# Kernel optimization log

Measured on AMD Instinct MI355X. Metric: run time of the kernel, lower is better.

The kernel has to match this reference:

```python
import jax, jax.numpy as jnp
import numpy as np

B, T, D = 512, 256, 64
LATENT = 128
H = 2 * LATENT  # hidden size = latent_dim * 2


def setup_inputs() -> dict:
    key = jax.random.key(0)
    ks = jax.random.split(key, 16)
    x = jax.random.normal(ks[0], (B, T, D), dtype=jnp.float32)
    # strictly increasing time points
    tps = jnp.cumsum(jax.random.uniform(ks[1], (T,), dtype=jnp.float32, minval=0.01, maxval=0.1))
    # ragged mask: each trajectory observed for a random prefix length in [1, T]
    lengths = jax.random.randint(ks[2], (B,), 1, T + 1)
    mask = (jnp.arange(T)[None, :] < lengths[:, None]).astype(jnp.float32)
    s = 0.05
    # GRUCell params (torch layout: gates ordered r, z, n)
    w_ih = jax.random.normal(ks[3], (3 * H, D), dtype=jnp.float32) * s
    w_hh = jax.random.normal(ks[4], (3 * H, H), dtype=jnp.float32) * s
    b_ih = jax.random.normal(ks[5], (3 * H,), dtype=jnp.float32) * s
    b_hh = jax.random.normal(ks[6], (3 * H,), dtype=jnp.float32) * s
    # Neural ODE func: Linear -> tanh -> Linear
    w1 = jax.random.normal(ks[7], (H, H), dtype=jnp.float32) * s
    b1 = jax.random.normal(ks[8], (H,), dtype=jnp.float32) * s
    w2 = jax.random.normal(ks[9], (H, H), dtype=jnp.float32) * s
    b2 = jax.random.normal(ks[10], (H,), dtype=jnp.float32) * s
    # output linear
    w_out = jax.random.normal(ks[11], (H, H), dtype=jnp.float32) * s
    b_out = jax.random.normal(ks[12], (H,), dtype=jnp.float32) * s
    return {"x": x, "tps": tps, "mask": mask, "w_ih": w_ih, "w_hh": w_hh,
            "b_ih": b_ih, "b_hh": b_hh, "w1": w1, "b1": b1, "w2": w2,
            "b2": b2, "w_out": w_out, "b_out": b_out}


def _gru_ode_forward(x, tps, mask, w_ih, w_hh, b_ih, b_hh, w1, b1, w2, b2, w_out, b_out):
    Bn, Tn, _ = x.shape
    # right_fill_mask: 1 wherever some earlier timestep (strictly before j) was observed
    r_fill = ((jnp.cumsum(mask, axis=1) - mask) > 0).astype(x.dtype)  # (B,T)
    # Euler dt per step; dt[0] is unused (r_fill[:,0]==0 forces h_ode=h at i=0)
    dt = jnp.diff(tps, prepend=tps[:1] - 0.01)  # (T,)

    def node_f(h):
        return jnp.tanh(h @ w1.T + b1) @ w2.T + b2

    def gru_cell(x_t, h):
        gi = x_t @ w_ih.T + b_ih
        gh = h @ w_hh.T + b_hh
        gi_r, gi_z, gi_n = jnp.split(gi, 3, axis=-1)
        gh_r, gh_z, gh_n = jnp.split(gh, 3, axis=-1)
        r = jax.nn.sigmoid(gi_r + gh_r)
        z = jax.nn.sigmoid(gi_z + gh_z)
        n = jnp.tanh(gi_n + r * gh_n)
        return (1.0 - z) * n + z * h

    def step(h, inp):
        x_t, dt_t, m_t, r_t = inp  # (B,D), (), (B,), (B,)
        h_euler = h + dt_t * node_f(h)          # single Euler step
        r_c = r_t[:, None]
        h_ode = h_euler * r_c + h * (1.0 - r_c)  # freeze state before first obs
        h_rnn = gru_cell(x_t, h_ode)
        m_c = m_t[:, None]
        h_new = h_rnn * m_c + h_ode * (1.0 - m_c)  # update only at observations
        return h_new, h_new

    h0 = jnp.zeros((Bn, H), dtype=x.dtype)
    xs = (jnp.swapaxes(x, 0, 1), dt, mask.T, r_fill.T)
    _, h_arr = jax.lax.scan(step, h0, xs)  # (T,B,H)
    # last observed timestep per trajectory
    ind = (Tn - 1) - jnp.argmax(mask[:, ::-1], axis=1)  # (B,)
    h_last = h_arr[ind, jnp.arange(Bn)]  # (B,H)
    return h_last @ w_out.T + b_out


def reference(x, tps, mask, w_ih, w_hh, b_ih, b_hh, w1, b1, w2, b2, w_out, b_out):
    return _gru_ode_forward(x, tps, mask, w_ih, w_hh, b_ih, b_hh, w1, b1, w2, b2, w_out, b_out)
```

## Files before the change

kernel.cpp:

```cpp
#include <hip/hip_runtime.h>
#include <hip/hip_bf16.h>


#define Bn 512
#define Tn 256
#define Dn 64
#define Hn 256

typedef __bf16 bf16x8 __attribute__((ext_vector_type(8)));
typedef float f32x4 __attribute__((ext_vector_type(4)));

__device__ __forceinline__ f32x4 mfma_bf16(bf16x8 a, bf16x8 b, f32x4 c) {
  return __builtin_amdgcn_mfma_f32_16x16x32_bf16(a, b, c, 0, 0, 0);
}
__device__ __forceinline__ float fast_sigmoid(float x) {
  return __builtin_amdgcn_rcpf(1.0f + __expf(-x));
}
__device__ __forceinline__ float fast_tanh(float x) {
  return 1.0f - 2.0f * __builtin_amdgcn_rcpf(1.0f + __expf(2.0f * x));
}

__global__ void pack_w(const float* __restrict__ w, __bf16* __restrict__ out,
                       int N, int K) {
  int idx = blockIdx.x * blockDim.x + threadIdx.x;
  if (idx >= N * K) return;
  int n = idx / K, k = idx % K;
  int tile = n >> 4, kb = k >> 5;
  int lane = (n & 15) + (((k & 31) >> 3) << 4);
  int j = k & 7;
  out[(((tile * (K >> 5) + kb) << 6) + lane) * 8 + j] = (__bf16)w[idx];
}

__global__ void pack_w_hilo(const float* __restrict__ w, __bf16* __restrict__ hi,
                            __bf16* __restrict__ lo, int N, int K) {
  int idx = blockIdx.x * blockDim.x + threadIdx.x;
  if (idx >= N * K) return;
  int n = idx / K, k = idx % K;
  int tile = n >> 4, kb = k >> 5;
  int lane = (n & 15) + (((k & 31) >> 3) << 4);
  int j = k & 7;
  int o = (((tile * (K >> 5) + kb) << 6) + lane) * 8 + j;
  float f = w[idx];
  __bf16 h = (__bf16)f;
  hi[o] = h;
  lo[o] = (__bf16)(f - (float)h);
}

__launch_bounds__(512)
__global__ void gru_ode_kernel(
    const float* __restrict__ x, const float* __restrict__ tps,
    const float* __restrict__ mask,
    const float* __restrict__ b_ih, const float* __restrict__ b_hh,
    const float* __restrict__ b1, const float* __restrict__ b2,
    const float* __restrict__ b_out,
    const __bf16* __restrict__ w1p, const __bf16* __restrict__ w2p,
    const __bf16* __restrict__ whhp, const __bf16* __restrict__ wihp,
    const __bf16* __restrict__ wouth, const __bf16* __restrict__ woutl,
    float* __restrict__ out) {
  __shared__ __align__(16) __bf16 h_fr[4096];
  __shared__ __align__(16) __bf16 a_fr[4096];
  __shared__ __align__(16) __bf16 o_fr[4096];
  __shared__ __align__(16) __bf16 wih_l[49152];
  __shared__ __align__(16) float hlast[16][260];
  __shared__ float tps_s[Tn];
  __shared__ int len_s[16];
  __shared__ int maxlen_s;

  const int tid = threadIdx.x;
  const int wv = tid >> 6;
  const int l = tid & 63;
  const int g = l >> 4;
  const int c = l & 15;
  const int m0 = blockIdx.x << 4;

  if (tid < Tn) tps_s[tid] = tps[tid];
#pragma unroll
  for (int i = 0; i < 8; i++) o_fr[tid + i * 512] = (__bf16)0.0f;
  {
    const int4* s4 = (const int4*)wihp;
    int4* d4 = (int4*)wih_l;
    for (int i = tid; i < 6144; i += 512) d4[i] = s4[i];
  }
  {
    int m = tid >> 5, l32 = tid & 31;
    const float* mr = mask + (size_t)(m0 + m) * Tn + l32 * 8;
    float s = 0.f;
#pragma unroll
    for (int i = 0; i < 8; i++) s += mr[i];
#pragma unroll
    for (int o = 16; o; o >>= 1) s += __shfl_down(s, o, 32);
    if (l32 == 0) len_s[m] = (int)(s + 0.5f);
  }
  __syncthreads();
  if (tid == 0) {
    int mx = 1;
    for (int i = 0; i < 16; i++) mx = max(mx, len_s[i]);
    maxlen_s = mx;
  }
  __syncthreads();
  const int maxlen = maxlen_s;
  int len4[4];
#pragma unroll
  for (int r = 0; r < 4; r++) len4[r] = len_s[4 * g + r];

  float bb1[2], bb2[2], brz[4], bin[2], bhn[2], bo[2];
#pragma unroll
  for (int nt = 0; nt < 2; nt++) {
    int col = 32 * wv + 16 * nt + c;
    bb1[nt] = b1[col];
    bb2[nt] = b2[col];
    brz[nt] = b_ih[col] + b_hh[col];
    brz[2 + nt] = b_ih[256 + col] + b_hh[256 + col];
    bin[nt] = b_ih[512 + col];
    bhn[nt] = b_hh[512 + col];
    bo[nt] = b_out[col];
  }

  float hreg[2][4] = {{0, 0, 0, 0}, {0, 0, 0, 0}};

  const bf16x8* w1f = (const bf16x8*)w1p;
  const bf16x8* w2f = (const bf16x8*)w2p;
  const bf16x8* whf = (const bf16x8*)whhp;
  const bf16x8* wif = (const bf16x8*)wih_l;

  const int wbase = (wv * 64 + 4 * g + 16 * (c >> 3)) * 8 + (c & 7);

  for (int t = 0; t < maxlen; t++) {
    const float* xp = x + (size_t)(m0 + c) * (Tn * Dn) + t * Dn + 8 * g;
    f32x4 xr0 = *(const f32x4*)(xp);
    f32x4 xr1 = *(const f32x4*)(xp + 4);
    f32x4 xr2 = *(const f32x4*)(xp + 32);
    f32x4 xr3 = *(const f32x4*)(xp + 36);

    if (t > 0) {
      bf16x8 hf[8];
#pragma unroll
      for (int kb = 0; kb < 8; kb++) hf[kb] = *(const bf16x8*)&h_fr[(kb * 64 + l) * 8];
#pragma unroll
      for (int nt = 0; nt < 2; nt++) {
        f32x4 acc = {0.f, 0.f, 0.f, 0.f};
#pragma unroll
        for (int kb = 0; kb < 8; kb++)
          acc = mfma_bf16(hf[kb], w1f[((2 * wv + nt) * 8 + kb) * 64 + l], acc);
#pragma unroll
        for (int r = 0; r < 4; r++)
          a_fr[wbase + (r + 32 * nt) * 8] = (__bf16)fast_tanh(acc[r] + bb1[nt]);
      }
      __syncthreads();
      float dtv = tps_s[t] - tps_s[t - 1];
      bf16x8 af[8];
#pragma unroll
      for (int kb = 0; kb < 8; kb++) af[kb] = *(const bf16x8*)&a_fr[(kb * 64 + l) * 8];
#pragma unroll
      for (int nt = 0; nt < 2; nt++) {
        f32x4 acc = {0.f, 0.f, 0.f, 0.f};
#pragma unroll
        for (int kb = 0; kb < 8; kb++)
          acc = mfma_bf16(af[kb], w2f[((2 * wv + nt) * 8 + kb) * 64 + l], acc);
#pragma unroll
        for (int r = 0; r < 4; r++) {
          hreg[nt][r] += dtv * (acc[r] + bb2[nt]);
          o_fr[wbase + (r + 32 * nt) * 8] = (__bf16)hreg[nt][r];
        }
      }
      __syncthreads();
    }
    bf16x8 of[8];
#pragma unroll
    for (int kb = 0; kb < 8; kb++) of[kb] = *(const bf16x8*)&o_fr[(kb * 64 + l) * 8];
    bf16x8 xf0, xf1;
#pragma unroll
    for (int j = 0; j < 4; j++) {
      xf0[j] = (__bf16)xr0[j]; xf0[4 + j] = (__bf16)xr1[j];
      xf1[j] = (__bf16)xr2[j]; xf1[4 + j] = (__bf16)xr3[j];
    }
    f32x4 arz[4], agi[2], agh[2];
#pragma unroll
    for (int q = 0; q < 4; q++) {
      int gate = q >> 1, nt = q & 1;
      int tile = (gate << 4) + 2 * wv + nt;
      f32x4 acc = {0.f, 0.f, 0.f, 0.f};
      acc = mfma_bf16(xf0, wif[(tile * 2 + 0) * 64 + l], acc);
      acc = mfma_bf16(xf1, wif[(tile * 2 + 1) * 64 + l], acc);
#pragma unroll
      for (int kb = 0; kb < 8; kb++)
        acc = mfma_bf16(of[kb], whf[(tile * 8 + kb) * 64 + l], acc);
      arz[q] = acc;
    }
#pragma unroll
    for (int nt = 0; nt < 2; nt++) {
      int tile = 32 + 2 * wv + nt;
      f32x4 ai = {0.f, 0.f, 0.f, 0.f}, ah = {0.f, 0.f, 0.f, 0.f};
      ai = mfma_bf16(xf0, wif[(tile * 2 + 0) * 64 + l], ai);
      ai = mfma_bf16(xf1, wif[(tile * 2 + 1) * 64 + l], ai);
#pragma unroll
      for (int kb = 0; kb < 8; kb++)
        ah = mfma_bf16(of[kb], whf[(tile * 8 + kb) * 64 + l], ah);
      agi[nt] = ai;
      agh[nt] = ah;
    }
#pragma unroll
    for (int nt = 0; nt < 2; nt++) {
#pragma unroll
      for (int r = 0; r < 4; r++) {
        float rg = fast_sigmoid(arz[nt][r] + brz[nt]);
        float zg = fast_sigmoid(arz[2 + nt][r] + brz[2 + nt]);
        float ng = fast_tanh(agi[nt][r] + bin[nt] + rg * (agh[nt][r] + bhn[nt]));
        float hn = (1.f - zg) * ng + zg * hreg[nt][r];
        hreg[nt][r] = hn;
        if (t == len4[r] - 1) hlast[4 * g + r][32 * wv + 16 * nt + c] = hn;
        h_fr[wbase + (r + 32 * nt) * 8] = (__bf16)hn;
      }
    }
    __syncthreads();
  }

  const bf16x8* woh = (const bf16x8*)wouth;
  const bf16x8* wol = (const bf16x8*)woutl;
  f32x4 oa[2] = {{0.f, 0.f, 0.f, 0.f}, {0.f, 0.f, 0.f, 0.f}};
#pragma unroll
  for (int kb = 0; kb < 8; kb++) {
    f32x4 v0 = *(const f32x4*)&hlast[c][kb * 32 + 8 * g];
    f32x4 v1 = *(const f32x4*)&hlast[c][kb * 32 + 8 * g + 4];
    bf16x8 hhi, hlo;
#pragma unroll
    for (int j = 0; j < 4; j++) {
      __bf16 p = (__bf16)v0[j]; hhi[j] = p; hlo[j] = (__bf16)(v0[j] - (float)p);
      __bf16 q = (__bf16)v1[j]; hhi[4 + j] = q; hlo[4 + j] = (__bf16)(v1[j] - (float)q);
    }
#pragma unroll
    for (int nt = 0; nt < 2; nt++) {
      int tile = 2 * wv + nt;
      oa[nt] = mfma_bf16(hhi, woh[(tile * 8 + kb) * 64 + l], oa[nt]);
      oa[nt] = mfma_bf16(hlo, woh[(tile * 8 + kb) * 64 + l], oa[nt]);
      oa[nt] = mfma_bf16(hhi, wol[(tile * 8 + kb) * 64 + l], oa[nt]);
    }
  }
#pragma unroll
  for (int nt = 0; nt < 2; nt++)
#pragma unroll
    for (int r = 0; r < 4; r++)
      out[(size_t)(m0 + 4 * g + r) * Hn + 32 * wv + 16 * nt + c] = oa[nt][r] + bo[nt];
}

extern "C" void kernel_launch(void* const* d_in, const int* in_sizes, int n_in,
                              void* d_out, int out_size, void* d_ws, size_t ws_size,
                              hipStream_t stream) {
  const float* x = (const float*)d_in[0];
  const float* tps = (const float*)d_in[1];
  const float* mask = (const float*)d_in[2];
  const float* w_ih = (const float*)d_in[3];
  const float* w_hh = (const float*)d_in[4];
  const float* b_ih = (const float*)d_in[5];
  const float* b_hh = (const float*)d_in[6];
  const float* w1 = (const float*)d_in[7];
  const float* b1 = (const float*)d_in[8];
  const float* w2 = (const float*)d_in[9];
  const float* b2 = (const float*)d_in[10];
  const float* w_out = (const float*)d_in[11];
  const float* b_out = (const float*)d_in[12];

  char* ws = (char*)d_ws;
  __bf16* w1p = (__bf16*)(ws + 0);
  __bf16* w2p = (__bf16*)(ws + 131072);
  __bf16* whhp = (__bf16*)(ws + 262144);
  __bf16* wihp = (__bf16*)(ws + 655360);
  __bf16* wouth = (__bf16*)(ws + 753664);
  __bf16* woutl = (__bf16*)(ws + 884736);

  pack_w<<<(256 * 256 + 255) / 256, 256, 0, stream>>>(w1, w1p, 256, 256);
  pack_w<<<(256 * 256 + 255) / 256, 256, 0, stream>>>(w2, w2p, 256, 256);
  pack_w<<<(768 * 256 + 255) / 256, 256, 0, stream>>>(w_hh, whhp, 768, 256);
  pack_w<<<(768 * 64 + 255) / 256, 256, 0, stream>>>(w_ih, wihp, 768, 64);
  pack_w_hilo<<<(256 * 256 + 255) / 256, 256, 0, stream>>>(w_out, wouth, woutl, 256, 256);

  gru_ode_kernel<<<32, 512, 0, stream>>>(x, tps, mask, b_ih, b_hh, b1, b2, b_out,
                                         w1p, w2p, whhp, wihp, wouth, woutl,
                                         (float*)d_out);
}
```

Measured before the change: 2.875 ms.

## Stream GRU weights through LDS ring via async global_load_lds, keep ODE weights in registers

Keeps W1/W2 fragments resident in registers instead of reloading them from global memory each step. W_hh and W_ih are streamed every timestep through a three-slot LDS ring using global_load_lds, with manual vmcnt waits. The x tile for the next step is prefetched into a double-buffered LDS buffer. Barriers are replaced with raw s_barrier plus lgkmcnt waits, and launch bounds request two blocks per CU. This trades heavier register pressure and fragile hand-written wait counts for overlapping the weight loads with MFMA work.

```diff
diff --git a/kernel.cpp b/kernel.cpp
--- a/kernel.cpp
+++ b/kernel.cpp
@@ -18,6 +18,11 @@
 }
 __device__ __forceinline__ float fast_tanh(float x) {
   return 1.0f - 2.0f * __builtin_amdgcn_rcpf(1.0f + __expf(2.0f * x));
+}
+
+__device__ __forceinline__ void gld16(const void* g, void* l) {
+  __builtin_amdgcn_global_load_lds((const __attribute__((address_space(1))) void*)g,
+                                   (__attribute__((address_space(3))) void*)l, 16, 0, 0);
 }
 
 __global__ void pack_w(const float* __restrict__ w, __bf16* __restrict__ out,
@@ -46,7 +51,43 @@
   lo[o] = (__bf16)(f - (float)h);
 }
 
-__launch_bounds__(512)
+#define RING_WAIT()                                          \
+  asm volatile("s_waitcnt vmcnt(8)" ::: "memory");           \
+  __builtin_amdgcn_sched_barrier(0);
+
+#define BAR()                                                \
+  asm volatile("s_waitcnt lgkmcnt(0)" ::: "memory");         \
+  __builtin_amdgcn_sched_barrier(0);                         \
+  __builtin_amdgcn_s_barrier();                              \
+  __builtin_amdgcn_sched_barrier(0);
+
+#define ISSUE_W(k)                                                             \
+  {                                                                            \
+    __bf16* db_ = slots + ((k) % 3) * 16384 + wv * 2048;                       \
+    if ((k) < 12) {                                                            \
+      const int tile_ = ((k) >> 2) * 16 + 2 * wv + (((k) & 3) >> 1);           \
+      const int kb0_ = ((k) & 1) * 4;                                          \
+      _Pragma("unroll") for (int f_ = 0; f_ < 4; f_++)                         \
+          gld16(whh_lane + (tile_ * 8 + kb0_ + f_) * 512, db_ + f_ * 512);     \
+    } else {                                                                   \
+      const int gg_ = (k) - 12;                                                \
+      _Pragma("unroll") for (int f_ = 0; f_ < 4; f_++) {                       \
+        const int tile_ = gg_ * 16 + 2 * wv + (f_ >> 1);                       \
+        gld16(wih_lane + (tile_ * 2 + (f_ & 1)) * 512, db_ + f_ * 512);        \
+      }                                                                        \
+    }                                                                          \
+  }
+
+#define ISSUE_X(tt)                                                            \
+  {                                                                            \
+    const int t2_ = ((tt) < Tn) ? (tt) : Tn - 1;                               \
+    const float* xs_ = x_lane + t2_ * 64;                                      \
+    float* xd_ = &xbuf[(tt) & 1][0];                                           \
+    _Pragma("unroll") for (int f_ = 0; f_ < 4; f_++)                           \
+        gld16(xs_ + f_ * 16, xd_ + f_ * 256);                                  \
+  }
+
+__launch_bounds__(512, 2)
 __global__ void gru_ode_kernel(
     const float* __restrict__ x, const float* __restrict__ tps,
     const float* __restrict__ mask,
@@ -57,12 +98,13 @@
     const __bf16* __restrict__ whhp, const __bf16* __restrict__ wihp,
     const __bf16* __restrict__ wouth, const __bf16* __restrict__ woutl,
     float* __restrict__ out) {
+  __shared__ __align__(16) __bf16 slots[49152];
   __shared__ __align__(16) __bf16 h_fr[4096];
   __shared__ __align__(16) __bf16 a_fr[4096];
   __shared__ __align__(16) __bf16 o_fr[4096];
-  __shared__ __align__(16) __bf16 wih_l[49152];
+  __shared__ __align__(16) float xbuf[2][1024];
   __shared__ __align__(16) float hlast[16][260];
-  __shared__ float tps_s[Tn];
+  __shared__ float dt_s[Tn];
   __shared__ int len_s[16];
   __shared__ int maxlen_s;
 
@@ -73,14 +115,9 @@
   const int c = l & 15;
   const int m0 = blockIdx.x << 4;
 
-  if (tid < Tn) tps_s[tid] = tps[tid];
+  if (tid < Tn) dt_s[tid] = tid ? tps[tid] - tps[tid - 1] : 0.01f;
 #pragma unroll
   for (int i = 0; i < 8; i++) o_fr[tid + i * 512] = (__bf16)0.0f;
-  {
-    const int4* s4 = (const int4*)wihp;
-    int4* d4 = (int4*)wih_l;
-    for (int i = tid; i < 6144; i += 512) d4[i] = s4[i];
-  }
   {
     int m = tid >> 5, l32 = tid & 31;
     const float* mr = mask + (size_t)(m0 + m) * Tn + l32 * 8;
@@ -116,103 +153,142 @@
     bo[nt] = b_out[col];
   }
 
+  bf16x8 w1f[2][8], w2f[2][8];
+#pragma unroll
+  for (int nt = 0; nt < 2; nt++)
+#pragma unroll
+    for (int kb = 0; kb < 8; kb++) {
+      w1f[nt][kb] = *(const bf16x8*)&w1p[(((2 * wv + nt) * 8 + kb) * 64 + l) * 8];
+      w2f[nt][kb] = *(const bf16x8*)&w2p[(((2 * wv + nt) * 8 + kb) * 64 + l) * 8];
+    }
+
   float hreg[2][4] = {{0, 0, 0, 0}, {0, 0, 0, 0}};
 
-  const bf16x8* w1f = (const bf16x8*)w1p;
-  const bf16x8* w2f = (const bf16x8*)w2p;
-  const bf16x8* whf = (const bf16x8*)whhp;
-  const bf16x8* wif = (const bf16x8*)wih_l;
+  const __bf16* whh_lane = whhp + l * 8;
+  const __bf16* wih_lane = wihp + l * 8;
+  const float* x_lane = x + (size_t)(m0 + (l & 15)) * (Tn * Dn) + (l >> 4) * 4;
 
   const int wbase = (wv * 64 + 4 * g + 16 * (c >> 3)) * 8 + (c & 7);
 
+  ISSUE_X(0);
+  asm volatile("s_waitcnt vmcnt(0)" ::: "memory");
+  __builtin_amdgcn_sched_barrier(0);
+  ISSUE_W(0);
+  ISSUE_W(1);
+  ISSUE_W(2);
+
+  bf16x8 xf0, xf1;
+
   for (int t = 0; t < maxlen; t++) {
-    const float* xp = x + (size_t)(m0 + c) * (Tn * Dn) + t * Dn + 8 * g;
-    f32x4 xr0 = *(const f32x4*)(xp);
-    f32x4 xr1 = *(const f32x4*)(xp + 4);
-    f32x4 xr2 = *(const f32x4*)(xp + 32);
-    f32x4 xr3 = *(const f32x4*)(xp + 36);
-
     if (t > 0) {
-      bf16x8 hf[8];
-#pragma unroll
-      for (int kb = 0; kb < 8; kb++) hf[kb] = *(const bf16x8*)&h_fr[(kb * 64 + l) * 8];
-#pragma unroll
-      for (int nt = 0; nt < 2; nt++) {
-        f32x4 acc = {0.f, 0.f, 0.f, 0.f};
+      {
+        bf16x8 hfv[8];
 #pragma unroll
         for (int kb = 0; kb < 8; kb++)
-          acc = mfma_bf16(hf[kb], w1f[((2 * wv + nt) * 8 + kb) * 64 + l], acc);
-#pragma unroll
-        for (int r = 0; r < 4; r++)
-          a_fr[wbase + (r + 32 * nt) * 8] = (__bf16)fast_tanh(acc[r] + bb1[nt]);
-      }
-      __syncthreads();
-      float dtv = tps_s[t] - tps_s[t - 1];
-      bf16x8 af[8];
-#pragma unroll
-      for (int kb = 0; kb < 8; kb++) af[kb] = *(const bf16x8*)&a_fr[(kb * 64 + l) * 8];
-#pragma unroll
-      for (int nt = 0; nt < 2; nt++) {
-        f32x4 acc = {0.f, 0.f, 0.f, 0.f};
+          hfv[kb] = *(const bf16x8*)&h_fr[(kb * 64 + l) * 8];
+#pragma unroll
+        for (int nt = 0; nt < 2; nt++) {
+          f32x4 acc = {0.f, 0.f, 0.f, 0.f};
+#pragma unroll
+          for (int kb = 0; kb < 8; kb++) acc = mfma_bf16(hfv[kb], w1f[nt][kb], acc);
+#pragma unroll
+          for (int r = 0; r < 4; r++)
+            a_fr[wbase + (r + 32 * nt) * 8] = (__bf16)fast_tanh(acc[r] + bb1[nt]);
+        }
+      }
+      BAR();
+      {
+        const float dtv = dt_s[t];
+        bf16x8 afv[8];
 #pragma unroll
         for (int kb = 0; kb < 8; kb++)
-          acc = mfma_bf16(af[kb], w2f[((2 * wv + nt) * 8 + kb) * 64 + l], acc);
-#pragma unroll
-        for (int r = 0; r < 4; r++) {
-          hreg[nt][r] += dtv * (acc[r] + bb2[nt]);
-          o_fr[wbase + (r + 32 * nt) * 8] = (__bf16)hreg[nt][r];
-        }
-      }
-      __syncthreads();
-    }
-    bf16x8 of[8];
-#pragma unroll
-    for (int kb = 0; kb < 8; kb++) of[kb] = *(const bf16x8*)&o_fr[(kb * 64 + l) * 8];
-    bf16x8 xf0, xf1;
-#pragma unroll
-    for (int j = 0; j < 4; j++) {
-      xf0[j] = (__bf16)xr0[j]; xf0[4 + j] = (__bf16)xr1[j];
-      xf1[j] = (__bf16)xr2[j]; xf1[4 + j] = (__bf16)xr3[j];
-    }
-    f32x4 arz[4], agi[2], agh[2];
-#pragma unroll
-    for (int q = 0; q < 4; q++) {
-      int gate = q >> 1, nt = q & 1;
-      int tile = (gate << 4) + 2 * wv + nt;
-      f32x4 acc = {0.f, 0.f, 0.f, 0.f};
-      acc = mfma_bf16(xf0, wif[(tile * 2 + 0) * 64 + l], acc);
-      acc = mfma_bf16(xf1, wif[(tile * 2 + 1) * 64 + l], acc);
-#pragma unroll
-      for (int kb = 0; kb < 8; kb++)
-        acc = mfma_bf16(of[kb], whf[(tile * 8 + kb) * 64 + l], acc);
-      arz[q] = acc;
-    }
+          afv[kb] = *(const bf16x8*)&a_fr[(kb * 64 + l) * 8];
+#pragma unroll
+        for (int nt = 0; nt < 2; nt++) {
+          f32x4 acc = {0.f, 0.f, 0.f, 0.f};
+#pragma unroll
+          for (int kb = 0; kb < 8; kb++) acc = mfma_bf16(afv[kb], w2f[nt][kb], acc);
+#pragma unroll
+          for (int r = 0; r < 4; r++) {
+            hreg[nt][r] += dtv * (acc[r] + bb2[nt]);
+            o_fr[wbase + (r + 32 * nt) * 8] = (__bf16)hreg[nt][r];
+          }
+        }
+      }
+      BAR();
+    }
+
+    f32x4 acc6[6], agi2[2];
+#pragma unroll
+    for (int q = 0; q < 6; q++) acc6[q] = (f32x4){0.f, 0.f, 0.f, 0.f};
+    agi2[0] = (f32x4){0.f, 0.f, 0.f, 0.f};
+    agi2[1] = (f32x4){0.f, 0.f, 0.f, 0.f};
+
+#pragma unroll
+    for (int p = 0; p < 16; p++) {
+      RING_WAIT();
+      if (p == 0) {
+        const float* xb = &xbuf[t & 1][0];
+        f32x4 a0 = *(const f32x4*)&xb[(2 * g) * 64 + c * 4];
+        f32x4 a1 = *(const f32x4*)&xb[(2 * g + 1) * 64 + c * 4];
+        f32x4 b0 = *(const f32x4*)&xb[(8 + 2 * g) * 64 + c * 4];
+        f32x4 b1v = *(const f32x4*)&xb[(9 + 2 * g) * 64 + c * 4];
+#pragma unroll
+        for (int j = 0; j < 4; j++) {
+          xf0[j] = (__bf16)a0[j];
+          xf0[4 + j] = (__bf16)a1[j];
+          xf1[j] = (__bf16)b0[j];
+          xf1[4 + j] = (__bf16)b1v[j];
+        }
+      }
+      if (p < 12) {
+        const int gate = p >> 2, nt = (p & 3) >> 1, kb0 = (p & 1) * 4;
+        const int ai = (gate < 2) ? gate * 2 + nt : 4 + nt;
+        const __bf16* sb = slots + (p % 3) * 16384 + wv * 2048 + l * 8;
+#pragma unroll
+        for (int f = 0; f < 4; f++) {
+          bf16x8 wf = *(const bf16x8*)(sb + f * 512);
+          bf16x8 ofr = *(const bf16x8*)&o_fr[((kb0 + f) * 64 + l) * 8];
+          acc6[ai] = mfma_bf16(ofr, wf, acc6[ai]);
+        }
+      } else if (p < 15) {
+        const int gg = p - 12;
+        const __bf16* sb = slots + (p % 3) * 16384 + wv * 2048 + l * 8;
+#pragma unroll
+        for (int f = 0; f < 4; f++) {
+          bf16x8 wf = *(const bf16x8*)(sb + f * 512);
+          if (gg < 2)
+            acc6[gg * 2 + (f >> 1)] = mfma_bf16((f & 1) ? xf1 : xf0, wf, acc6[gg * 2 + (f >> 1)]);
+          else
+            agi2[f >> 1] = mfma_bf16((f & 1) ? xf1 : xf0, wf, agi2[f >> 1]);
+        }
+      }
+      asm volatile("s_waitcnt lgkmcnt(0)" ::: "memory");
+      __builtin_amdgcn_sched_barrier(0);
+      {
+        const int k = (p + 3) & 15;
+        if (k == 15) {
+          ISSUE_X(t + 1);
+        } else {
+          ISSUE_W(k);
+        }
+      }
+    }
+
 #pragma unroll
     for (int nt = 0; nt < 2; nt++) {
-      int tile = 32 + 2 * wv + nt;
-      f32x4 ai = {0.f, 0.f, 0.f, 0.f}, ah = {0.f, 0.f, 0.f, 0.f};
-      ai = mfma_bf16(xf0, wif[(tile * 2 + 0) * 64 + l], ai);
-      ai = mfma_bf16(xf1, wif[(tile * 2 + 1) * 64 + l], ai);
-#pragma unroll
-      for (int kb = 0; kb < 8; kb++)
-        ah = mfma_bf16(of[kb], whf[(tile * 8 + kb) * 64 + l], ah);
-      agi[nt] = ai;
-      agh[nt] = ah;
-    }
-#pragma unroll
-    for (int nt = 0; nt < 2; nt++) {
 #pragma unroll
       for (int r = 0; r < 4; r++) {
-        float rg = fast_sigmoid(arz[nt][r] + brz[nt]);
-        float zg = fast_sigmoid(arz[2 + nt][r] + brz[2 + nt]);
-        float ng = fast_tanh(agi[nt][r] + bin[nt] + rg * (agh[nt][r] + bhn[nt]));
+        float rg = fast_sigmoid(acc6[nt][r] + brz[nt]);
+        float zg = fast_sigmoid(acc6[2 + nt][r] + brz[2 + nt]);
+        float ng = fast_tanh(agi2[nt][r] + bin[nt] + rg * (acc6[4 + nt][r] + bhn[nt]));
         float hn = (1.f - zg) * ng + zg * hreg[nt][r];
         hreg[nt][r] = hn;
         if (t == len4[r] - 1) hlast[4 * g + r][32 * wv + 16 * nt + c] = hn;
         h_fr[wbase + (r + 32 * nt) * 8] = (__bf16)hn;
       }
     }
-    __syncthreads();
+    BAR();
   }
 
   const bf16x8* woh = (const bf16x8*)wouth;
```

Measured after the change: 2.666 ms. -7.3%, faster.

## Hold ODE weights in registers and double-buffer W_hh prefetch in GRU step

Applied to the files above, without the earlier changes.

Loads the w1/w2 ODE weight fragments into registers once before the time loop instead of fetching them from global memory every step. The recurrent W_hh fragments are streamed in 4-fragment chunks with double-buffered prefetch, so the global loads overlap the MFMA accumulation. __syncthreads is replaced by a custom LDS-wait-plus-barrier macro, dt is precomputed, and launch bounds now request 2 blocks per CU. The cost is much higher register pressure, which may cause spills or lower occupancy.

```diff
diff --git a/kernel.cpp b/kernel.cpp
--- a/kernel.cpp
+++ b/kernel.cpp
@@ -46,7 +46,23 @@
   lo[o] = (__bf16)(f - (float)h);
 }
 
-__launch_bounds__(512)
+#define BAR()                                        \
+  asm volatile("s_waitcnt lgkmcnt(0)" ::: "memory"); \
+  __builtin_amdgcn_sched_barrier(0);                 \
+  __builtin_amdgcn_s_barrier();                      \
+  __builtin_amdgcn_sched_barrier(0);
+
+#define CHUNK_Q(p) (((p) >= 6) ? (p) - 6 : (p))
+#define CHUNK_TILE(p) (((CHUNK_Q(p) >> 1) << 4) + 2 * wv + (CHUNK_Q(p) & 1))
+#define CHUNK_KB0(p) (((p) >= 6) ? 4 : 0)
+#define ISSUE_CHUNK(p, b)                                                  \
+  {                                                                        \
+    const int tl_ = CHUNK_TILE(p), kb_ = CHUNK_KB0(p);                     \
+    _Pragma("unroll") for (int f_ = 0; f_ < 4; f_++)                       \
+        wb[b][f_] = whf[(tl_ * 8 + kb_ + f_) * 64 + l];                    \
+  }
+
+__launch_bounds__(512, 2)
 __global__ void gru_ode_kernel(
     const float* __restrict__ x, const float* __restrict__ tps,
     const float* __restrict__ mask,
@@ -57,12 +73,12 @@
     const __bf16* __restrict__ whhp, const __bf16* __restrict__ wihp,
     const __bf16* __restrict__ wouth, const __bf16* __restrict__ woutl,
     float* __restrict__ out) {
+  __shared__ __align__(16) __bf16 wih_l[49152];
   __shared__ __align__(16) __bf16 h_fr[4096];
   __shared__ __align__(16) __bf16 a_fr[4096];
   __shared__ __align__(16) __bf16 o_fr[4096];
-  __shared__ __align__(16) __bf16 wih_l[49152];
   __shared__ __align__(16) float hlast[16][260];
-  __shared__ float tps_s[Tn];
+  __shared__ float dt_s[Tn];
   __shared__ int len_s[16];
   __shared__ int maxlen_s;
 
@@ -73,7 +89,7 @@
   const int c = l & 15;
   const int m0 = blockIdx.x << 4;
 
-  if (tid < Tn) tps_s[tid] = tps[tid];
+  if (tid < Tn) dt_s[tid] = tid ? tps[tid] - tps[tid - 1] : 0.01f;
 #pragma unroll
   for (int i = 0; i < 8; i++) o_fr[tid + i * 512] = (__bf16)0.0f;
   {
@@ -116,103 +132,130 @@
     bo[nt] = b_out[col];
   }
 
+  bf16x8 w1f[2][8], w2f[2][8];
+#pragma unroll
+  for (int nt = 0; nt < 2; nt++)
+#pragma unroll
+    for (int kb = 0; kb < 8; kb++) {
+      w1f[nt][kb] = *(const bf16x8*)&w1p[(((2 * wv + nt) * 8 + kb) * 64 + l) * 8];
+      w2f[nt][kb] = *(const bf16x8*)&w2p[(((2 * wv + nt) * 8 + kb) * 64 + l) * 8];
+    }
+
   float hreg[2][4] = {{0, 0, 0, 0}, {0, 0, 0, 0}};
 
-  const bf16x8* w1f = (const bf16x8*)w1p;
-  const bf16x8* w2f = (const bf16x8*)w2p;
   const bf16x8* whf = (const bf16x8*)whhp;
-  const bf16x8* wif = (const bf16x8*)wih_l;
+  const bf16x8* wifl = (const bf16x8*)wih_l;
+  const float* xrow = x + (size_t)(m0 + c) * (Tn * Dn) + 8 * g;
 
   const int wbase = (wv * 64 + 4 * g + 16 * (c >> 3)) * 8 + (c & 7);
 
   for (int t = 0; t < maxlen; t++) {
-    const float* xp = x + (size_t)(m0 + c) * (Tn * Dn) + t * Dn + 8 * g;
+    const float* xp = xrow + t * Dn;
     f32x4 xr0 = *(const f32x4*)(xp);
     f32x4 xr1 = *(const f32x4*)(xp + 4);
     f32x4 xr2 = *(const f32x4*)(xp + 32);
     f32x4 xr3 = *(const f32x4*)(xp + 36);
+    bf16x8 wb[2][4];
+    ISSUE_CHUNK(0, 0);
+    ISSUE_CHUNK(1, 1);
 
     if (t > 0) {
-      bf16x8 hf[8];
-#pragma unroll
-      for (int kb = 0; kb < 8; kb++) hf[kb] = *(const bf16x8*)&h_fr[(kb * 64 + l) * 8];
-#pragma unroll
-      for (int nt = 0; nt < 2; nt++) {
-        f32x4 acc = {0.f, 0.f, 0.f, 0.f};
+      {
+        bf16x8 hfv[8];
 #pragma unroll
         for (int kb = 0; kb < 8; kb++)
-          acc = mfma_bf16(hf[kb], w1f[((2 * wv + nt) * 8 + kb) * 64 + l], acc);
-#pragma unroll
-        for (int r = 0; r < 4; r++)
-          a_fr[wbase + (r + 32 * nt) * 8] = (__bf16)fast_tanh(acc[r] + bb1[nt]);
-      }
-      __syncthreads();
-      float dtv = tps_s[t] - tps_s[t - 1];
-      bf16x8 af[8];
-#pragma unroll
-      for (int kb = 0; kb < 8; kb++) af[kb] = *(const bf16x8*)&a_fr[(kb * 64 + l) * 8];
-#pragma unroll
-      for (int nt = 0; nt < 2; nt++) {
-        f32x4 acc = {0.f, 0.f, 0.f, 0.f};
+          hfv[kb] = *(const bf16x8*)&h_fr[(kb * 64 + l) * 8];
+#pragma unroll
+        for (int nt = 0; nt < 2; nt++) {
+          f32x4 acc = {0.f, 0.f, 0.f, 0.f};
+#pragma unroll
+          for (int kb = 0; kb < 8; kb++) acc = mfma_bf16(hfv[kb], w1f[nt][kb], acc);
+#pragma unroll
+          for (int r = 0; r < 4; r++)
+            a_fr[wbase + (r + 32 * nt) * 8] = (__bf16)fast_tanh(acc[r] + bb1[nt]);
+        }
+      }
+      BAR();
+      {
+        const float dtv = dt_s[t];
+        bf16x8 afv[8];
 #pragma unroll
         for (int kb = 0; kb < 8; kb++)
-          acc = mfma_bf16(af[kb], w2f[((2 * wv + nt) * 8 + kb) * 64 + l], acc);
-#pragma unroll
-        for (int r = 0; r < 4; r++) {
-          hreg[nt][r] += dtv * (acc[r] + bb2[nt]);
-          o_fr[wbase + (r + 32 * nt) * 8] = (__bf16)hreg[nt][r];
+          afv[kb] = *(const bf16x8*)&a_fr[(kb * 64 + l) * 8];
+#pragma unroll
+        for (int nt = 0; nt < 2; nt++) {
+          f32x4 acc = {0.f, 0.f, 0.f, 0.f};
+#pragma unroll
+          for (int kb = 0; kb < 8; kb++) acc = mfma_bf16(afv[kb], w2f[nt][kb], acc);
+#pragma unroll
+          for (int r = 0; r < 4; r++) {
+            hreg[nt][r] += dtv * (acc[r] + bb2[nt]);
+            o_fr[wbase + (r + 32 * nt) * 8] = (__bf16)hreg[nt][r];
+          }
         }
       }
-      __syncthreads();
-    }
-    bf16x8 of[8];
-#pragma unroll
-    for (int kb = 0; kb < 8; kb++) of[kb] = *(const bf16x8*)&o_fr[(kb * 64 + l) * 8];
+      BAR();
+    }
+
     bf16x8 xf0, xf1;
 #pragma unroll
     for (int j = 0; j < 4; j++) {
-      xf0[j] = (__bf16)xr0[j]; xf0[4 + j] = (__bf16)xr1[j];
-      xf1[j] = (__bf16)xr2[j]; xf1[4 + j] = (__bf16)xr3[j];
-    }
-    f32x4 arz[4], agi[2], agh[2];
-#pragma unroll
-    for (int q = 0; q < 4; q++) {
-      int gate = q >> 1, nt = q & 1;
-      int tile = (gate << 4) + 2 * wv + nt;
-      f32x4 acc = {0.f, 0.f, 0.f, 0.f};
-      acc = mfma_bf16(xf0, wif[(tile * 2 + 0) * 64 + l], acc);
-      acc = mfma_bf16(xf1, wif[(tile * 2 + 1) * 64 + l], acc);
-#pragma unroll
-      for (int kb = 0; kb < 8; kb++)
-        acc = mfma_bf16(of[kb], whf[(tile * 8 + kb) * 64 + l], acc);
-      arz[q] = acc;
-    }
+      xf0[j] = (__bf16)xr0[j];
+      xf0[4 + j] = (__bf16)xr1[j];
+      xf1[j] = (__bf16)xr2[j];
+      xf1[4 + j] = (__bf16)xr3[j];
+    }
+    f32x4 acc6[6], agi2[2];
+#pragma unroll
+    for (int q = 0; q < 6; q++) acc6[q] = (f32x4){0.f, 0.f, 0.f, 0.f};
+    agi2[0] = (f32x4){0.f, 0.f, 0.f, 0.f};
+    agi2[1] = (f32x4){0.f, 0.f, 0.f, 0.f};
+
+    bf16x8 ofv[4];
+#pragma unroll
+    for (int p = 0; p < 12; p++) {
+      const int kb0 = CHUNK_KB0(p);
+      const int q = CHUNK_Q(p);
+      const int gate = q >> 1, nt = q & 1;
+      if (p == 0 || p == 6) {
+#pragma unroll
+        for (int f = 0; f < 4; f++)
+          ofv[f] = *(const bf16x8*)&o_fr[((kb0 + f) * 64 + l) * 8];
+      }
+      f32x4& accr = (gate == 0) ? acc6[nt] : (gate == 1) ? acc6[2 + nt] : acc6[4 + nt];
+#pragma unroll
+      for (int f = 0; f < 4; f++) accr = mfma_bf16(ofv[f], wb[p & 1][f], accr);
+      if (p < 10) {
+        ISSUE_CHUNK(p + 2, p & 1);
+      }
+    }
+#pragma unroll
+    for (int gg = 0; gg < 3; gg++) {
+#pragma unroll
+      for (int f = 0; f < 4; f++) {
+        const int tile = gg * 16 + 2 * wv + (f >> 1);
+        bf16x8 wf = wifl[(tile * 2 + (f & 1)) * 64 + l];
+        if (gg < 2)
+          acc6[gg * 2 + (f >> 1)] = mfma_bf16((f & 1) ? xf1 : xf0, wf, acc6[gg * 2 + (f >> 1)]);
+        else
+          agi2[f >> 1] = mfma_bf16((f & 1) ? xf1 : xf0, wf, agi2[f >> 1]);
+      }
+    }
+
 #pragma unroll
     for (int nt = 0; nt < 2; nt++) {
-      int tile = 32 + 2 * wv + nt;
-      f32x4 ai = {0.f, 0.f, 0.f, 0.f}, ah = {0.f, 0.f, 0.f, 0.f};
-      ai = mfma_bf16(xf0, wif[(tile * 2 + 0) * 64 + l], ai);
-      ai = mfma_bf16(xf1, wif[(tile * 2 + 1) * 64 + l], ai);
-#pragma unroll
-      for (int kb = 0; kb < 8; kb++)
-        ah = mfma_bf16(of[kb], whf[(tile * 8 + kb) * 64 + l], ah);
-      agi[nt] = ai;
-      agh[nt] = ah;
-    }
-#pragma unroll
-    for (int nt = 0; nt < 2; nt++) {
 #pragma unroll
       for (int r = 0; r < 4; r++) {
-        float rg = fast_sigmoid(arz[nt][r] + brz[nt]);
-        float zg = fast_sigmoid(arz[2 + nt][r] + brz[2 + nt]);
-        float ng = fast_tanh(agi[nt][r] + bin[nt] + rg * (agh[nt][r] + bhn[nt]));
+        float rg = fast_sigmoid(acc6[nt][r] + brz[nt]);
+        float zg = fast_sigmoid(acc6[2 + nt][r] + brz[2 + nt]);
+        float ng = fast_tanh(agi2[nt][r] + bin[nt] + rg * (acc6[4 + nt][r] + bhn[nt]));
         float hn = (1.f - zg) * ng + zg * hreg[nt][r];
         hreg[nt][r] = hn;
         if (t == len4[r] - 1) hlast[4 * g + r][32 * wv + 16 * nt + c] = hn;
         h_fr[wbase + (r + 32 * nt) * 8] = (__bf16)hn;
       }
     }
-    __syncthreads();
+    BAR();
   }
 
   const bf16x8* woh = (const bf16x8*)wouth;
```

New measurement: 2.723 ms. 1.06x faster.
